# Performance work log

Hardware: AMD Instinct MI355X
Metric: run time of the kernel (lower is better)

Reference implementation:

```python
import jax, jax.numpy as jnp
import numpy as np
from jax import lax

BN_EPS = 1e-3  # keras BatchNormalization default

def _conv(x, w):
    # x: (N,H,W,Cin), w: (kh,kw,Cin,Cout), 'same' padding, stride 1
    return lax.conv_general_dilated(x, w, (1, 1), 'SAME',
                                    dimension_numbers=('NHWC', 'HWIO', 'NHWC'))

def _hard_sigmoid(x):  # keras ConvLSTM2D default recurrent_activation
    return jnp.clip(0.2 * x + 0.5, 0.0, 1.0)

def _convlstm(x, Wx, Wh, b, return_sequences):
    # x: (B,T,H,W,Cin); Wx: (3,3,Cin,4F); Wh: (3,3,F,4F); gates order i,f,c,o
    B, T, H, W, Cin = x.shape
    F = Wh.shape[2]
    # precompute input-to-gate convs for all timesteps at once (one big conv)
    gx = _conv(x.reshape(B * T, H, W, Cin), Wx) + b
    gx = gx.reshape(B, T, H, W, 4 * F).transpose(1, 0, 2, 3, 4)  # (T,B,H,W,4F)
    h0 = jnp.zeros((B, H, W, F), x.dtype)
    c0 = jnp.zeros((B, H, W, F), x.dtype)

    def step(carry, gxt):
        h, c = carry
        z = gxt + _conv(h, Wh)
        zi, zf, zc, zo = jnp.split(z, 4, axis=-1)
        c = _hard_sigmoid(zf) * c + _hard_sigmoid(zi) * jnp.tanh(zc)
        h = _hard_sigmoid(zo) * jnp.tanh(c)
        return (h, c), h

    (hT, _), hs = lax.scan(step, (h0, c0), gx)
    if return_sequences:
        return hs.transpose(1, 0, 2, 3, 4)  # (B,T,H,W,F)
    return hT  # (B,H,W,F)

def _bn(x, gamma, beta, mean, var):
    return (x - mean) * (gamma * lax.rsqrt(var + BN_EPS)) + beta

def _pool_thw(x):  # MaxPool3D(pool_size=(1,2,2))
    B, T, H, W, C = x.shape
    return x.reshape(B, T, H // 2, 2, W // 2, 2, C).max(axis=(3, 5))

def _pool_hw(x):  # MaxPool2D()
    B, H, W, C = x.shape
    return x.reshape(B, H // 2, 2, W // 2, 2, C).max(axis=(2, 4))

def setup_inputs() -> dict:
    key = jax.random.key(0)
    ks = jax.random.split(key, 16)
    s = 0.05  # weight scale
    d = {
        'x':   jax.random.normal(ks[0], (8, 12, 64, 64, 3), jnp.float32),
        'W1x': jax.random.normal(ks[1], (3, 3, 3, 64), jnp.float32) * s,
        'W1h': jax.random.normal(ks[2], (3, 3, 16, 64), jnp.float32) * s,
        'b1':  jnp.zeros((64,), jnp.float32),
        'g1':  jnp.ones((16,), jnp.float32),
        'be1': jnp.zeros((16,), jnp.float32),
        'm1':  jax.random.normal(ks[3], (16,), jnp.float32) * 0.1,
        'v1':  jax.random.uniform(ks[4], (16,), jnp.float32) + 0.5,
        'W2x': jax.random.normal(ks[5], (3, 3, 16, 128), jnp.float32) * s,
        'W2h': jax.random.normal(ks[6], (3, 3, 32, 128), jnp.float32) * s,
        'b2':  jnp.zeros((128,), jnp.float32),
        'g2':  jnp.ones((32,), jnp.float32),
        'be2': jnp.zeros((32,), jnp.float32),
        'm2':  jax.random.normal(ks[7], (32,), jnp.float32) * 0.1,
        'v2':  jax.random.uniform(ks[8], (32,), jnp.float32) + 0.5,
        'W3x': jax.random.normal(ks[9], (3, 3, 32, 256), jnp.float32) * s,
        'W3h': jax.random.normal(ks[10], (3, 3, 64, 256), jnp.float32) * s,
        'b3':  jnp.zeros((256,), jnp.float32),
        'Wd1': jax.random.normal(ks[11], (4096, 10000), jnp.float32) * 0.01,
        'bd1': jnp.zeros((10000,), jnp.float32),
        'Wd2': jax.random.normal(ks[12], (10000, 1000), jnp.float32) * 0.01,
        'bd2': jnp.zeros((1000,), jnp.float32),
        'Wd3': jax.random.normal(ks[13], (1000, 100), jnp.float32) * 0.03,
        'bd3': jnp.zeros((100,), jnp.float32),
        'Wd4': jax.random.normal(ks[14], (100, 10), jnp.float32) * 0.1,
        'bd4': jnp.zeros((10,), jnp.float32),
        'Wc':  jax.random.normal(ks[15], (10, 1), jnp.float32) * 0.3,
        'bc':  jnp.zeros((1,), jnp.float32),
    }
    return d

def reference(x, W1x, W1h, b1, g1, be1, m1, v1,
              W2x, W2h, b2, g2, be2, m2, v2,
              W3x, W3h, b3,
              Wd1, bd1, Wd2, bd2, Wd3, bd3, Wd4, bd4, Wc, bc):
    h = _convlstm(x, W1x, W1h, b1, True)          # (B,12,64,64,16)
    h = _bn(h, g1, be1, m1, v1)
    h = _pool_thw(h)                              # (B,12,32,32,16)
    h = _convlstm(h, W2x, W2h, b2, True)          # (B,12,32,32,32)
    h = _bn(h, g2, be2, m2, v2)
    h = _pool_thw(h)                              # (B,12,16,16,32)
    h = _convlstm(h, W3x, W3h, b3, False)         # (B,16,16,64)
    h = _pool_hw(h)                               # (B,8,8,64)
    h = h.reshape(h.shape[0], -1)                 # (B,4096)
    h = h @ Wd1 + bd1
    h = h @ Wd2 + bd2
    h = h @ Wd3 + bd3
    h = h @ Wd4 + bd4
    return h @ Wc + bc                            # (B,1)
```

## Files before the change

### kernel.cpp

```cpp
#include <hip/hip_runtime.h>
#include <hip/hip_bf16.h>
#include <math.h>

template<int H, int W, int Cin, int Cout, int TH, int TW>
__global__ __launch_bounds__(256) void conv3x3_bias(
    const float* __restrict__ in, const float* __restrict__ wt,
    const float* __restrict__ bias, float* __restrict__ out, int NB)
{
  constexpr int TILES_X = W / TW, TILES_Y = H / TH;
  constexpr int PAD_W = TW + 2, PAD_H = TH + 2;
  constexpr int LDS_N = PAD_H * PAD_W * Cin;
  __shared__ __align__(16) float tile[LDS_N];

  int blk = blockIdx.x;
  int n = blk / (TILES_X * TILES_Y);
  int trem = blk % (TILES_X * TILES_Y);
  int ty = trem / TILES_X, tx = trem % TILES_X;
  int y0 = ty * TH, x0 = tx * TW;
  const float* inN = in + (size_t)n * H * W * Cin;

  for (int i = threadIdx.x; i < LDS_N; i += 256) {
    int ci = i % Cin; int rem = i / Cin;
    int xx = rem % PAD_W; int yy = rem / PAD_W;
    int gy = y0 + yy - 1, gx = x0 + xx - 1;
    float v = 0.f;
    if (gy >= 0 && gy < H && gx >= 0 && gx < W)
      v = inN[((size_t)gy * W + gx) * Cin + ci];
    tile[i] = v;
  }
  __syncthreads();

  constexpr int P = TH * TW;
  constexpr int PPT = P / 4;
  int lane_co = threadIdx.x & 63;
  int wv = threadIdx.x >> 6;
  float* outN = out + (size_t)n * H * W * Cout;

  int cc = blockIdx.y * 64;
  {
    int co = cc + lane_co;
    float acc[PPT];
    float bco = bias[co];
#pragma unroll
    for (int j = 0; j < PPT; ++j) acc[j] = bco;

#pragma unroll
    for (int kh = 0; kh < 3; ++kh)
#pragma unroll
    for (int kw = 0; kw < 3; ++kw) {
      const float* wtap = wt + ((size_t)(kh * 3 + kw) * Cin) * Cout + co;
      if constexpr (Cin % 4 == 0) {
#pragma unroll 1
        for (int c4 = 0; c4 < Cin; c4 += 4) {
          float w0 = wtap[(size_t)(c4 + 0) * Cout];
          float w1 = wtap[(size_t)(c4 + 1) * Cout];
          float w2 = wtap[(size_t)(c4 + 2) * Cout];
          float w3 = wtap[(size_t)(c4 + 3) * Cout];
#pragma unroll
          for (int j = 0; j < PPT; ++j) {
            int p = wv * PPT + j;
            int ly = p / TW, lx = p % TW;
            const float4 h4 = *(const float4*)&tile[((ly + kh) * PAD_W + (lx + kw)) * Cin + c4];
            acc[j] += h4.x * w0 + h4.y * w1 + h4.z * w2 + h4.w * w3;
          }
        }
      } else {
#pragma unroll 1
        for (int c1 = 0; c1 < Cin; ++c1) {
          float w0 = wtap[(size_t)c1 * Cout];
#pragma unroll
          for (int j = 0; j < PPT; ++j) {
            int p = wv * PPT + j;
            int ly = p / TW, lx = p % TW;
            acc[j] += tile[((ly + kh) * PAD_W + (lx + kw)) * Cin + c1] * w0;
          }
        }
      }
    }
#pragma unroll
    for (int j = 0; j < PPT; ++j) {
      int p = wv * PPT + j;
      int ly = p / TW, lx = p % TW;
      outN[((size_t)(y0 + ly) * W + (x0 + lx)) * Cout + co] = acc[j];
    }
  }
}

__device__ __forceinline__ float hsig(float x) {
  return fminf(fmaxf(0.2f * x + 0.5f, 0.f), 1.f);
}

template<int H, int W, int F, int TH, int TW>
__global__ __launch_bounds__(256) void lstm_step(
    const float* __restrict__ gx, long gx_bstride,
    const float* __restrict__ hprev, long hp_bstride,
    const float* __restrict__ wh,
    float* __restrict__ c,
    float* __restrict__ hout, long ho_bstride,
    int first)
{
  constexpr int TILES_X = W / TW, TILES_Y = H / TH;
  constexpr int PAD_W = TW + 2, PAD_H = TH + 2;
  constexpr int LDS_N = PAD_H * PAD_W * F;
  __shared__ __align__(16) float tile[LDS_N];

  int blk = blockIdx.x;
  int b = blk / (TILES_X * TILES_Y);
  int trem = blk % (TILES_X * TILES_Y);
  int ty = trem / TILES_X, tx = trem % TILES_X;
  int y0 = ty * TH, x0 = tx * TW;

  if (first) {
    for (int i = threadIdx.x; i < LDS_N; i += 256) tile[i] = 0.f;
  } else {
    const float* hb = hprev + (size_t)b * hp_bstride;
    for (int i = threadIdx.x; i < LDS_N; i += 256) {
      int ci = i % F; int rem = i / F;
      int xx = rem % PAD_W, yy = rem / PAD_W;
      int gy = y0 + yy - 1, gxp = x0 + xx - 1;
      float v = 0.f;
      if (gy >= 0 && gy < H && gxp >= 0 && gxp < W)
        v = hb[((size_t)gy * W + gxp) * F + ci];
      tile[i] = v;
    }
  }
  __syncthreads();

  constexpr int G = 256 / F;
  constexpr int P = TH * TW;
  constexpr int NP = P / G;
  int f = threadIdx.x % F;
  int pg = threadIdx.x / F;

  float acc[4][NP];
  const float* gxb = gx + (size_t)b * gx_bstride;
#pragma unroll
  for (int j = 0; j < NP; ++j) {
    int p = pg * NP + j;
    int gy = y0 + p / TW, gxp = x0 + p % TW;
    size_t base = ((size_t)gy * W + gxp) * 4 * F;
#pragma unroll
    for (int g = 0; g < 4; ++g) acc[g][j] = gxb[base + g * F + f];
  }

#pragma unroll
  for (int kh = 0; kh < 3; ++kh)
#pragma unroll
  for (int kw = 0; kw < 3; ++kw) {
    const float* wtap = wh + ((size_t)(kh * 3 + kw) * F) * 4 * F + f;
#pragma unroll 1
    for (int c4 = 0; c4 < F; c4 += 4) {
      float4 h4[NP];
#pragma unroll
      for (int j = 0; j < NP; ++j) {
        int p = pg * NP + j;
        int ly = p / TW, lx = p % TW;
        h4[j] = *(const float4*)&tile[((ly + kh) * PAD_W + (lx + kw)) * F + c4];
      }
      const float* wc0 = wtap + (size_t)c4 * 4 * F;
#pragma unroll
      for (int g = 0; g < 4; ++g) {
        float w0 = wc0[(size_t)g * F];
        float w1 = wc0[(size_t)4 * F + g * F];
        float w2 = wc0[(size_t)8 * F + g * F];
        float w3 = wc0[(size_t)12 * F + g * F];
#pragma unroll
        for (int j = 0; j < NP; ++j)
          acc[g][j] += h4[j].x * w0 + h4[j].y * w1 + h4[j].z * w2 + h4[j].w * w3;
      }
    }
  }

  float* cb = c + (size_t)b * H * W * F;
  float* hb2 = hout + (size_t)b * ho_bstride;
#pragma unroll
  for (int j = 0; j < NP; ++j) {
    int p = pg * NP + j;
    int gy = y0 + p / TW, gxp = x0 + p % TW;
    size_t idx = ((size_t)gy * W + gxp) * F + f;
    float zi = acc[0][j], zf = acc[1][j], zc = acc[2][j], zo = acc[3][j];
    float cold = first ? 0.f : cb[idx];
    float cn = hsig(zf) * cold + hsig(zi) * tanhf(zc);
    cb[idx] = cn;
    hb2[idx] = hsig(zo) * tanhf(cn);
  }
}

__global__ void bnpool_kernel(const float* __restrict__ in,
                              const float* __restrict__ g, const float* __restrict__ be,
                              const float* __restrict__ m, const float* __restrict__ v,
                              float* __restrict__ out, int total, int H, int W, int F)
{
  int i = blockIdx.x * 256 + threadIdx.x;
  if (i >= total) return;
  int f = i % F; int rem = i / F;
  int x = rem % (W / 2); rem /= (W / 2);
  int y = rem % (H / 2); int nt = rem / (H / 2);
  float scale = g[f] * rsqrtf(v[f] + 1e-3f);
  float shift = be[f] - m[f] * scale;
  const float* base = in + (((size_t)nt * H + 2 * y) * W + 2 * x) * F + f;
  float a0 = base[0] * scale + shift;
  float a1 = base[F] * scale + shift;
  float a2 = base[(size_t)W * F] * scale + shift;
  float a3 = base[(size_t)W * F + F] * scale + shift;
  out[i] = fmaxf(fmaxf(a0, a1), fmaxf(a2, a3));
}

__global__ void poolhw_kernel(const float* __restrict__ in, float* __restrict__ out, int total)
{
  int i = blockIdx.x * 256 + threadIdx.x;
  if (i >= total) return;
  int f = i % 64; int rem = i / 64;
  int x = rem % 8; rem /= 8;
  int y = rem % 8; int b = rem / 8;
  const float* base = in + (((size_t)b * 16 + 2 * y) * 16 + 2 * x) * 64 + f;
  float a0 = base[0], a1 = base[64], a2 = base[16 * 64], a3 = base[16 * 64 + 64];
  out[i] = fmaxf(fmaxf(a0, a1), fmaxf(a2, a3));
}

__global__ __launch_bounds__(256) void dense_partial(
    const float* __restrict__ x, const float* __restrict__ w,
    float* __restrict__ part, int K, int N, int kchunk)
{
  extern __shared__ __align__(16) float xs[];
  int kb = blockIdx.y;
  int k0 = kb * kchunk;
  int klen = min(kchunk, K - k0);
  for (int i = threadIdx.x; i < klen * 8; i += 256) {
    int kk = i >> 3, b = i & 7;
    xs[i] = x[(size_t)b * K + k0 + kk];
  }
  __syncthreads();
  int co = blockIdx.x * 256 + threadIdx.x;
  if (co >= N) return;
  float acc[8];
#pragma unroll
  for (int b = 0; b < 8; ++b) acc[b] = 0.f;
  const float4* xs4 = (const float4*)xs;
  const float* wp = w + (size_t)k0 * N + co;
#pragma unroll 4
  for (int kk = 0; kk < klen; ++kk) {
    float wv = wp[(size_t)kk * N];
    float4 lo = xs4[kk * 2], hi = xs4[kk * 2 + 1];
    acc[0] += lo.x * wv; acc[1] += lo.y * wv;
    acc[2] += lo.z * wv; acc[3] += lo.w * wv;
    acc[4] += hi.x * wv; acc[5] += hi.y * wv;
    acc[6] += hi.z * wv; acc[7] += hi.w * wv;
  }
#pragma unroll
  for (int b = 0; b < 8; ++b)
    part[((size_t)kb * 8 + b) * N + co] = acc[b];
}

__global__ __launch_bounds__(256) void dense_reduce(
    const float* __restrict__ part, const float* __restrict__ bias,
    float* __restrict__ out, int N, int S)
{
  int co = blockIdx.x * 256 + threadIdx.x;
  int b = blockIdx.y;
  if (co >= N) return;
  float acc = bias[co];
#pragma unroll 4
  for (int kb = 0; kb < S; ++kb)
    acc += part[((size_t)kb * 8 + b) * N + co];
  out[(size_t)b * N + co] = acc;
}

__global__ void dense_part(const float* __restrict__ x, const float* __restrict__ w,
                           const float* __restrict__ bias, float* __restrict__ out,
                           int K, int N, int kchunk)
{
  extern __shared__ float xs[];
  int co = blockIdx.x * 256 + threadIdx.x;
  int kb = blockIdx.y;
  int k0 = kb * kchunk;
  int k1 = min(k0 + kchunk, K);
  int klen = k1 - k0;
  for (int i = threadIdx.x; i < klen * 8; i += 256) {
    int b = i / klen; int kk = i % klen;
    xs[b * kchunk + kk] = x[(size_t)b * K + k0 + kk];
  }
  __syncthreads();
  if (co >= N) return;
  float acc[8];
#pragma unroll
  for (int b = 0; b < 8; ++b) acc[b] = 0.f;
#pragma unroll 1
  for (int k = k0; k < k1; ++k) {
    float wv = w[(size_t)k * N + co];
    int kk = k - k0;
#pragma unroll
    for (int b = 0; b < 8; ++b) acc[b] += xs[b * kchunk + kk] * wv;
  }
  float bi = (kb == 0) ? bias[co] : 0.f;
#pragma unroll
  for (int b = 0; b < 8; ++b) atomicAdd(&out[(size_t)b * N + co], acc[b] + bi);
}

__global__ void dense_tail(const float* __restrict__ d3,
                           const float* __restrict__ w4, const float* __restrict__ b4,
                           const float* __restrict__ wc, const float* __restrict__ bc,
                           float* __restrict__ out)
{
  __shared__ float d4[8][10];
  int t = threadIdx.x;
  if (t < 80) {
    int b = t / 10, co = t % 10;
    float acc = b4[co];
    for (int k = 0; k < 100; ++k) acc += d3[b * 100 + k] * w4[k * 10 + co];
    d4[b][co] = acc;
  }
  __syncthreads();
  if (t < 8) {
    float acc = bc[0];
    for (int j = 0; j < 10; ++j) acc += d4[t][j] * wc[j];
    out[t] = acc;
  }
}

extern "C" void kernel_launch(void* const* d_in, const int* in_sizes, int n_in,
                              void* d_out, int out_size, void* d_ws, size_t ws_size,
                              hipStream_t stream)
{
  const float* x   = (const float*)d_in[0];
  const float* W1x = (const float*)d_in[1];
  const float* W1h = (const float*)d_in[2];
  const float* b1  = (const float*)d_in[3];
  const float* g1  = (const float*)d_in[4];
  const float* be1 = (const float*)d_in[5];
  const float* m1  = (const float*)d_in[6];
  const float* v1  = (const float*)d_in[7];
  const float* W2x = (const float*)d_in[8];
  const float* W2h = (const float*)d_in[9];
  const float* b2  = (const float*)d_in[10];
  const float* g2  = (const float*)d_in[11];
  const float* be2 = (const float*)d_in[12];
  const float* m2  = (const float*)d_in[13];
  const float* v2  = (const float*)d_in[14];
  const float* W3x = (const float*)d_in[15];
  const float* W3h = (const float*)d_in[16];
  const float* b3  = (const float*)d_in[17];
  const float* Wd1 = (const float*)d_in[18];
  const float* bd1 = (const float*)d_in[19];
  const float* Wd2 = (const float*)d_in[20];
  const float* bd2 = (const float*)d_in[21];
  const float* Wd3 = (const float*)d_in[22];
  const float* bd3 = (const float*)d_in[23];
  const float* Wd4 = (const float*)d_in[24];
  const float* bd4 = (const float*)d_in[25];
  const float* Wc  = (const float*)d_in[26];
  const float* bc  = (const float*)d_in[27];

  char* ws = (char*)d_ws;
  size_t off = 0;
  auto alloc = [&](size_t bytes) { size_t r = off; off = (off + bytes + 255) & ~(size_t)255; return r; };
  size_t oR0   = alloc(100663296);
  size_t oR1   = alloc(25165824);
  size_t oR2   = alloc(6291456);
  size_t oR3   = alloc(2097152);
  size_t oh3a  = alloc(524288);
  size_t oh3b  = alloc(524288);
  size_t oflat = alloc(131072);
  size_t od1   = alloc(320000);
  size_t od2   = alloc(32000);
  size_t od3   = alloc(3200);
  (void)ws_size; (void)in_sizes; (void)n_in; (void)out_size;

  float* gx1   = (float*)(ws + oR0);
  float* gx2   = (float*)(ws + oR0);
  float* gx3   = (float*)(ws + oR0);
  float* part1 = (float*)(ws + oR0);
  float* part2 = (float*)(ws + oR0 + 33554432);
  float* hseq1 = (float*)(ws + oR1);
  float* hseq2 = (float*)(ws + oR1);
  float* pool1 = (float*)(ws + oR2);
  float* pool2 = (float*)(ws + oR2);
  float* cbuf  = (float*)(ws + oR3);
  float* h3a   = (float*)(ws + oh3a);
  float* h3b   = (float*)(ws + oh3b);
  float* flat  = (float*)(ws + oflat);
  float* d1    = (float*)(ws + od1);
  float* d2    = (float*)(ws + od2);
  float* d3b   = (float*)(ws + od3);

  const int B = 8, T = 12;

  conv3x3_bias<64, 64, 3, 64, 8, 8><<<dim3(96 * 64, 1), 256, 0, stream>>>(x, W1x, b1, gx1, 96);
  {
    const long gxs = (long)T * 64 * 64 * 64;
    const long hs  = (long)T * 64 * 64 * 16;
    for (int t = 0; t < T; ++t) {
      lstm_step<64, 64, 16, 8, 8><<<B * 64, 256, 0, stream>>>(
          gx1 + (size_t)t * 64 * 64 * 64, gxs,
          t ? hseq1 + (size_t)(t - 1) * 64 * 64 * 16 : nullptr, hs,
          W1h, cbuf, hseq1 + (size_t)t * 64 * 64 * 16, hs, t == 0);
    }
  }
  {
    int total = B * T * 32 * 32 * 16;
    bnpool_kernel<<<(total + 255) / 256, 256, 0, stream>>>(hseq1, g1, be1, m1, v1, pool1, total, 64, 64, 16);
  }

  conv3x3_bias<32, 32, 16, 128, 8, 8><<<dim3(96 * 16, 2), 256, 0, stream>>>(pool1, W2x, b2, gx2, 96);
  {
    const long gxs = (long)T * 32 * 32 * 128;
    const long hs  = (long)T * 32 * 32 * 32;
    for (int t = 0; t < T; ++t) {
      lstm_step<32, 32, 32, 4, 4><<<B * 64, 256, 0, stream>>>(
          gx2 + (size_t)t * 32 * 32 * 128, gxs,
          t ? hseq2 + (size_t)(t - 1) * 32 * 32 * 32 : nullptr, hs,
          W2h, cbuf, hseq2 + (size_t)t * 32 * 32 * 32, hs, t == 0);
    }
  }
  {
    int total = B * T * 16 * 16 * 32;
    bnpool_kernel<<<(total + 255) / 256, 256, 0, stream>>>(hseq2, g2, be2, m2, v2, pool2, total, 32, 32, 32);
  }

  conv3x3_bias<16, 16, 32, 256, 8, 8><<<dim3(96 * 4, 4), 256, 0, stream>>>(pool2, W3x, b3, gx3, 96);
  {
    const long gxs = (long)T * 16 * 16 * 256;
    const long hs  = (long)16 * 16 * 64;
    for (int t = 0; t < T; ++t) {
      float* hout = (t % 2 == 0) ? h3a : h3b;
      const float* hp = (t % 2 == 0) ? h3b : h3a;
      lstm_step<16, 16, 64, 2, 4><<<B * 32, 256, 0, stream>>>(
          gx3 + (size_t)t * 16 * 16 * 256, gxs,
          t ? hp : nullptr, hs,
          W3h, cbuf, hout, hs, t == 0);
    }
  }
  poolhw_kernel<<<(32768 + 255) / 256, 256, 0, stream>>>(h3b, flat, 32768);

  dense_partial<<<dim3(40, 64), 256, 64 * 8 * 4, stream>>>(flat, Wd1, part1, 4096, 10000, 64);
  dense_reduce<<<dim3(40, 8), 256, 0, stream>>>(part1, bd1, d1, 10000, 64);
  dense_partial<<<dim3(4, 125), 256, 80 * 8 * 4, stream>>>(d1, Wd2, part2, 10000, 1000, 80);
  dense_reduce<<<dim3(4, 8), 256, 0, stream>>>(part2, bd2, d2, 1000, 125);
  hipMemsetAsync(d3b, 0, 3200, stream);
  dense_part<<<dim3(1, 8), 256, 8 * 128 * 4, stream>>>(d2, Wd3, bd3, d3b, 1000, 100, 128);
  dense_tail<<<1, 128, 0, stream>>>(d3b, Wd4, bd4, Wc, bc, (float*)d_out);
}
```

Baseline: 1.580 ms.

## Register-block conv over multiple output-channel groups and shrink LSTM step tiles

The input conv kernel now has each thread hold accumulators for several output-channel groups. This reuses every LDS float4 load across NG channels, covers all of Cout in one block instead of splitting it across blockIdx.y, and pads Cin to a multiple of 4 so the Cin=3 layer also uses vector loads. Spatial tiles shrink to 4x8. The LSTM step kernels for layers 1 and 3 use smaller tiles, doubling the grid size to raise parallelism. The cost is more registers per thread and more halo redundancy per block.

```diff
diff --git a/kernel.cpp b/kernel.cpp
--- a/kernel.cpp
+++ b/kernel.cpp
@@ -2,14 +2,18 @@
 #include <hip/hip_bf16.h>
 #include <math.h>
 
-template<int H, int W, int Cin, int Cout, int TH, int TW>
+template<int H, int W, int Cin, int Cout, int TH, int TW, int COL, int NG>
 __global__ __launch_bounds__(256) void conv3x3_bias(
     const float* __restrict__ in, const float* __restrict__ wt,
-    const float* __restrict__ bias, float* __restrict__ out, int NB)
-{
+    const float* __restrict__ bias, float* __restrict__ out)
+{
+  static_assert(COL * NG == Cout, "cout coverage");
+  constexpr int CIN_P = (Cin % 4 == 0) ? Cin : ((Cin + 3) / 4) * 4;
   constexpr int TILES_X = W / TW, TILES_Y = H / TH;
   constexpr int PAD_W = TW + 2, PAD_H = TH + 2;
-  constexpr int LDS_N = PAD_H * PAD_W * Cin;
+  constexpr int LDS_N = PAD_H * PAD_W * CIN_P;
+  constexpr int NPG = 256 / COL;
+  constexpr int PPT = TH * TW / NPG;
   __shared__ __align__(16) float tile[LDS_N];
 
   int blk = blockIdx.x;
@@ -20,69 +24,62 @@
   const float* inN = in + (size_t)n * H * W * Cin;
 
   for (int i = threadIdx.x; i < LDS_N; i += 256) {
-    int ci = i % Cin; int rem = i / Cin;
+    int ci = i % CIN_P; int rem = i / CIN_P;
     int xx = rem % PAD_W; int yy = rem / PAD_W;
     int gy = y0 + yy - 1, gx = x0 + xx - 1;
     float v = 0.f;
-    if (gy >= 0 && gy < H && gx >= 0 && gx < W)
+    if (ci < Cin && gy >= 0 && gy < H && gx >= 0 && gx < W)
       v = inN[((size_t)gy * W + gx) * Cin + ci];
     tile[i] = v;
   }
   __syncthreads();
 
-  constexpr int P = TH * TW;
-  constexpr int PPT = P / 4;
-  int lane_co = threadIdx.x & 63;
-  int wv = threadIdx.x >> 6;
+  int cobase = threadIdx.x % COL;
+  int pg = threadIdx.x / COL;
   float* outN = out + (size_t)n * H * W * Cout;
 
-  int cc = blockIdx.y * 64;
-  {
-    int co = cc + lane_co;
-    float acc[PPT];
-    float bco = bias[co];
-#pragma unroll
-    for (int j = 0; j < PPT; ++j) acc[j] = bco;
-
-#pragma unroll
-    for (int kh = 0; kh < 3; ++kh)
-#pragma unroll
-    for (int kw = 0; kw < 3; ++kw) {
-      const float* wtap = wt + ((size_t)(kh * 3 + kw) * Cin) * Cout + co;
-      if constexpr (Cin % 4 == 0) {
+  float acc[NG][PPT];
+#pragma unroll
+  for (int g = 0; g < NG; ++g) {
+    float bco = bias[g * COL + cobase];
+#pragma unroll
+    for (int j = 0; j < PPT; ++j) acc[g][j] = bco;
+  }
+
+#pragma unroll
+  for (int kh = 0; kh < 3; ++kh)
+#pragma unroll
+  for (int kw = 0; kw < 3; ++kw) {
+    const float* wtap = wt + ((size_t)(kh * 3 + kw) * Cin) * Cout + cobase;
 #pragma unroll 1
-        for (int c4 = 0; c4 < Cin; c4 += 4) {
-          float w0 = wtap[(size_t)(c4 + 0) * Cout];
-          float w1 = wtap[(size_t)(c4 + 1) * Cout];
-          float w2 = wtap[(size_t)(c4 + 2) * Cout];
-          float w3 = wtap[(size_t)(c4 + 3) * Cout];
-#pragma unroll
-          for (int j = 0; j < PPT; ++j) {
-            int p = wv * PPT + j;
-            int ly = p / TW, lx = p % TW;
-            const float4 h4 = *(const float4*)&tile[((ly + kh) * PAD_W + (lx + kw)) * Cin + c4];
-            acc[j] += h4.x * w0 + h4.y * w1 + h4.z * w2 + h4.w * w3;
-          }
+    for (int c4 = 0; c4 < CIN_P; c4 += 4) {
+      float w[NG][4];
+#pragma unroll
+      for (int g = 0; g < NG; ++g)
+#pragma unroll
+        for (int ch = 0; ch < 4; ++ch) {
+          w[g][ch] = (Cin % 4 == 0 || c4 + ch < Cin)
+                         ? wtap[(size_t)(c4 + ch) * Cout + g * COL] : 0.f;
         }
-      } else {
-#pragma unroll 1
-        for (int c1 = 0; c1 < Cin; ++c1) {
-          float w0 = wtap[(size_t)c1 * Cout];
-#pragma unroll
-          for (int j = 0; j < PPT; ++j) {
-            int p = wv * PPT + j;
-            int ly = p / TW, lx = p % TW;
-            acc[j] += tile[((ly + kh) * PAD_W + (lx + kw)) * Cin + c1] * w0;
-          }
-        }
+#pragma unroll
+      for (int j = 0; j < PPT; ++j) {
+        int p = pg * PPT + j;
+        int ly = p / TW, lx = p % TW;
+        const float4 h4 = *(const float4*)&tile[((ly + kh) * PAD_W + (lx + kw)) * CIN_P + c4];
+#pragma unroll
+        for (int g = 0; g < NG; ++g)
+          acc[g][j] += h4.x * w[g][0] + h4.y * w[g][1] + h4.z * w[g][2] + h4.w * w[g][3];
       }
     }
-#pragma unroll
-    for (int j = 0; j < PPT; ++j) {
-      int p = wv * PPT + j;
-      int ly = p / TW, lx = p % TW;
-      outN[((size_t)(y0 + ly) * W + (x0 + lx)) * Cout + co] = acc[j];
-    }
+  }
+
+#pragma unroll
+  for (int j = 0; j < PPT; ++j) {
+    int p = pg * PPT + j;
+    int ly = p / TW, lx = p % TW;
+    float* op = &outN[((size_t)(y0 + ly) * W + (x0 + lx)) * Cout + cobase];
+#pragma unroll
+    for (int g = 0; g < NG; ++g) op[g * COL] = acc[g][j];
   }
 }
 
@@ -385,12 +382,12 @@
 
   const int B = 8, T = 12;
 
-  conv3x3_bias<64, 64, 3, 64, 8, 8><<<dim3(96 * 64, 1), 256, 0, stream>>>(x, W1x, b1, gx1, 96);
+  conv3x3_bias<64, 64, 3, 64, 4, 8, 32, 2><<<96 * 128, 256, 0, stream>>>(x, W1x, b1, gx1);
   {
     const long gxs = (long)T * 64 * 64 * 64;
     const long hs  = (long)T * 64 * 64 * 16;
     for (int t = 0; t < T; ++t) {
-      lstm_step<64, 64, 16, 8, 8><<<B * 64, 256, 0, stream>>>(
+      lstm_step<64, 64, 16, 4, 8><<<B * 128, 256, 0, stream>>>(
           gx1 + (size_t)t * 64 * 64 * 64, gxs,
           t ? hseq1 + (size_t)(t - 1) * 64 * 64 * 16 : nullptr, hs,
           W1h, cbuf, hseq1 + (size_t)t * 64 * 64 * 16, hs, t == 0);
@@ -401,7 +398,7 @@
     bnpool_kernel<<<(total + 255) / 256, 256, 0, stream>>>(hseq1, g1, be1, m1, v1, pool1, total, 64, 64, 16);
   }
 
-  conv3x3_bias<32, 32, 16, 128, 8, 8><<<dim3(96 * 16, 2), 256, 0, stream>>>(pool1, W2x, b2, gx2, 96);
+  conv3x3_bias<32, 32, 16, 128, 4, 8, 32, 4><<<96 * 32, 256, 0, stream>>>(pool1, W2x, b2, gx2);
   {
     const long gxs = (long)T * 32 * 32 * 128;
     const long hs  = (long)T * 32 * 32 * 32;
@@ -417,14 +414,14 @@
     bnpool_kernel<<<(total + 255) / 256, 256, 0, stream>>>(hseq2, g2, be2, m2, v2, pool2, total, 32, 32, 32);
   }
 
-  conv3x3_bias<16, 16, 32, 256, 8, 8><<<dim3(96 * 4, 4), 256, 0, stream>>>(pool2, W3x, b3, gx3, 96);
+  conv3x3_bias<16, 16, 32, 256, 4, 8, 64, 4><<<96 * 8, 256, 0, stream>>>(pool2, W3x, b3, gx3);
   {
     const long gxs = (long)T * 16 * 16 * 256;
     const long hs  = (long)16 * 16 * 64;
     for (int t = 0; t < T; ++t) {
       float* hout = (t % 2 == 0) ? h3a : h3b;
       const float* hp = (t % 2 == 0) ? h3b : h3a;
-      lstm_step<16, 16, 64, 2, 4><<<B * 32, 256, 0, stream>>>(
+      lstm_step<16, 16, 64, 2, 2><<<B * 64, 256, 0, stream>>>(
           gx3 + (size_t)t * 16 * 16 * 256, gxs,
           t ? hp : nullptr, hs,
           W3h, cbuf, hout, hs, t == 0);
```

Measured after the change: 1.640 ms. +3.8%, slower.
